# Kernel optimization log

Measured on AMD Instinct MI355X. Metric: run time of the kernel, lower is better.

The kernel has to match this reference:

```python
import jax, jax.numpy as jnp
import numpy as np

B, L = 32, 64
VOCAB, EMB, HID, MEM, NVAL = 32000, 256, 512, 256, 1024
NSLOTS, KTOP = 4096, 16
DEQ_ITERS, RELAX = 8, 0.5
DECAY, MEM_SCALE = 0.997, 1.0
HIDDEN = 1024  # max(128, 2*HID)


def _norm(x):
    # torch F.normalize: x / max(||x||, eps)
    return x / jnp.maximum(jnp.linalg.norm(x, axis=-1, keepdims=True), 1e-12)


def setup_inputs() -> dict:
    key = jax.random.key(0)
    ks = jax.random.split(key, 20)
    def gn(k, shape, scale):
        return jax.random.normal(k, shape, jnp.float32) * scale
    inp = {}
    inp['tokens'] = jax.random.randint(ks[0], (B, L), 0, VOCAB)
    inp['key_ids'] = jax.random.randint(ks[1], (B,), 0, NVAL)
    inp['write_pos'] = jax.random.randint(ks[2], (B,), 0, L // 2)
    inp['query_pos'] = jax.random.randint(ks[3], (B,), L // 2, L)
    inp['value_ids'] = jax.random.randint(ks[4], (B,), 0, NVAL)
    inp['embed_W'] = gn(ks[5], (VOCAB, EMB), 1.0)
    inp['key_W'] = gn(ks[6], (NVAL, MEM), 0.1)
    inp['value_W'] = gn(ks[7], (NVAL, MEM), 0.1)
    din = HID + EMB + MEM
    inp['u_W1'] = gn(ks[8], (din, HIDDEN), din ** -0.5)
    inp['u_b1'] = jnp.zeros((HIDDEN,), jnp.float32)
    inp['u_W2'] = gn(ks[9], (HIDDEN, HID), HIDDEN ** -0.5)
    inp['u_b2'] = jnp.zeros((HID,), jnp.float32)
    inp['l_Wi'] = gn(ks[10], (HID, HID), HID ** -0.5)
    inp['l_Wh'] = gn(ks[11], (HID, HID), HID ** -0.5)
    inp['l_b'] = jnp.zeros((HID,), jnp.float32)
    inp['l_Wti'] = gn(ks[12], (HID, HID), HID ** -0.5)
    inp['l_Wth'] = gn(ks[13], (HID, HID), HID ** -0.5)
    inp['l_bt'] = jnp.zeros((HID,), jnp.float32)
    inp['h0'] = jnp.zeros((HID,), jnp.float32)
    inp['z2v_W'] = gn(ks[14], (2 * HID, MEM), (2 * HID) ** -0.5)
    inp['z2v_b'] = jnp.zeros((MEM,), jnp.float32)
    inp['logit_scale_raw'] = jnp.asarray(2.0, jnp.float32)
    inp['slot_keys'] = _norm(gn(ks[15], (NSLOTS, MEM), 1.0))
    return inp


def _forward(tokens, key_ids, write_pos, query_pos, embed_W, key_W, value_W,
             u_W1, u_b1, u_W2, u_b2, l_Wi, l_Wh, l_b, l_Wti, l_Wth, l_bt,
             h0, z2v_W, z2v_b, logit_scale_raw, slot_keys):
    scale = jax.nn.softplus(logit_scale_raw) + 1e-3
    V_proto = _norm(value_W)                              # [NVAL, MEM]
    # Memory ops are non-differentiable in the original (detach + no_grad writes)
    kv = jax.lax.stop_gradient(_norm(key_W[key_ids]))     # [B, MEM]
    sk = jax.lax.stop_gradient(slot_keys)                 # [NSLOTS, MEM]

    x_seq = jnp.swapaxes(embed_W[tokens], 0, 1)           # [L, B, EMB]
    t_idx = jnp.arange(L)
    mw_seq = t_idx[:, None] == write_pos[None, :]         # [L, B]
    mq_seq = t_idx[:, None] == query_pos[None, :]         # [L, B]

    # Slot addressing depends only on the (fixed per-sequence) key vectors,
    # so the top-k slot selection can be hoisted out of the time loop.
    top_s, top_i = jax.lax.top_k(kv @ sk.T, KTOP)         # [B, KTOP]
    w_slot = jax.nn.softmax(top_s, axis=-1)               # [B, KTOP]

    def mem_read(M):
        return jnp.einsum('bk,bkd->bd', w_slot, M[top_i])  # gather [B,KTOP,MEM]

    def mem_write(M, vals, mask):
        wm = w_slot * mask[:, None].astype(M.dtype)
        contrib = jnp.zeros_like(M).at[top_i.reshape(-1)].add(
            (wm[..., None] * vals[:, None, :]).reshape(-1, MEM))
        decay_t = jnp.where(mask.any(), DECAY, 1.0)       # decay only on write events
        return decay_t * M + contrib

    def step(carry, xs):
        z, h, M, lm, lp = carry
        x_t, mw, mq = xs
        # mem_into_deq: non-diff memory read is injected only at query steps
        v_t = mem_read(M) * mq[:, None].astype(x_t.dtype) * MEM_SCALE
        # DEQ: damped fixed-point iteration z <- (1-r) z + r f(z)
        for _ in range(DEQ_ITERS):
            inp = jnp.concatenate([z, x_t, v_t], axis=-1)
            f = z + jnp.tanh(inp @ u_W1 + u_b1) @ u_W2 + u_b2
            z = (1.0 - RELAX) * z + RELAX * f
        # Liquid cell: time-constant gated relaxation toward tanh candidate
        g = jnp.tanh(z @ l_Wi + h @ l_Wh + l_b)
        tau = jax.nn.softplus(z @ l_Wti + h @ l_Wth + l_bt) + 1.0
        h = h + (g - h) / tau
        v_pred = _norm(jnp.concatenate([z, h], axis=-1) @ z2v_W + z2v_b)
        M = mem_write(M, jax.lax.stop_gradient(v_pred), mw)
        v_mem = mem_read(M)
        lm = jnp.where(mq[:, None], scale * (_norm(v_mem) @ V_proto.T), lm)
        lp = jnp.where(mq[:, None], scale * (v_pred @ V_proto.T), lp)
        return (z, h, M, lm, lp), None

    z0 = jnp.zeros((B, HID), jnp.float32)
    h_init = jnp.broadcast_to(h0, (B, HID))
    M0 = jnp.zeros((NSLOTS, MEM), jnp.float32)
    lm0 = jnp.zeros((B, NVAL), jnp.float32)
    lp0 = jnp.zeros((B, NVAL), jnp.float32)
    carry, _ = jax.lax.scan(step, (z0, h_init, M0, lm0, lp0), (x_seq, mw_seq, mq_seq))
    return carry[3]  # logits_main [B, NVAL]


def reference(tokens, key_ids, write_pos, query_pos, value_ids, embed_W, key_W,
              value_W, u_W1, u_b1, u_W2, u_b2, l_Wi, l_Wh, l_b, l_Wti, l_Wth,
              l_bt, h0, z2v_W, z2v_b, logit_scale_raw, slot_keys):
    # value_ids only feeds auxiliary losses in the original; logits_main does not use it.
    return _forward(tokens, key_ids, write_pos, query_pos, embed_W, key_W, value_W,
                    u_W1, u_b1, u_W2, u_b2, l_Wi, l_Wh, l_b, l_Wti, l_Wth, l_bt,
                    h0, z2v_W, z2v_b, logit_scale_raw, slot_keys)
```

## Files before the change

### kernel.cpp

```cpp
#include <hip/hip_runtime.h>
#include <math.h>


#define NGRP 8
#define WPG  32

#define OF_SCALE  0
#define OF_DFAC   32
#define OF_RNV    64
#define OF_TOPW   1088
#define OF_SCORES 1600
#define OF_Z      132672
#define OF_CP     198208
#define OF_G      230976
#define OF_TAU    247360
#define OF_H      263744
#define OF_ZS     280128
#define OF_HS     296512
#define OF_M      312896
#define OF_W1ZT   1361472
#define OF_W1XT   1885760
#define OF_W2T    2147904
#define OF_LWIT   2672192
#define OF_LWHT   2934336
#define OF_LWTIT  3196480
#define OF_LWTHT  3458624

__device__ __forceinline__ float softplusf_(float x){ return x > 20.f ? x : log1pf(expf(x)); }

__device__ __forceinline__ float cldf(const float* p){
  return __hip_atomic_load(p, __ATOMIC_RELAXED, __HIP_MEMORY_SCOPE_AGENT);
}
__device__ __forceinline__ void cstf(float* p, float v){
  __hip_atomic_store(p, v, __ATOMIC_RELAXED, __HIP_MEMORY_SCOPE_AGENT);
}

__device__ __forceinline__ void lbar(int* flags, int w, int& epoch){
  asm volatile("s_waitcnt vmcnt(0)" ::: "memory");
  __syncthreads();
  epoch++;
  if (threadIdx.x == 0)
    __hip_atomic_store(&flags[w], epoch, __ATOMIC_RELAXED, __HIP_MEMORY_SCOPE_AGENT);
  if (threadIdx.x < 32){
    while (__hip_atomic_load(&flags[threadIdx.x], __ATOMIC_RELAXED,
                             __HIP_MEMORY_SCOPE_AGENT) < epoch)
      __builtin_amdgcn_s_sleep(1);
  }
  asm volatile("" ::: "memory");
  __syncthreads();
}

__global__ void __launch_bounds__(256) emma_tr(const float* src, float* dst,
                                               int shift, int total)
{
  const int R = total >> shift;
  const int cmask = (1 << shift) - 1;
  for (int idx = blockIdx.x*256 + threadIdx.x; idx < total; idx += gridDim.x*256){
    int r = idx >> shift, c = idx & cmask;
    dst[(size_t)c * R + r] = src[idx];
  }
}

__global__ void __launch_bounds__(256) emma_k1a(
    const int* key_ids, const int* write_pos,
    const float* key_W, const float* value_W, const float* slot_keys,
    const float* lsr, int* wsI, float* wsF)
{
  const int wg = blockIdx.x, tid = threadIdx.x;
  if (wg < 256) {
    const int b = wg >> 3, chunk = wg & 7;
    __shared__ __align__(16) float s_kv[256];
    __shared__ float red[256];
    float v = key_W[key_ids[b]*256 + tid];
    red[tid] = v*v; __syncthreads();
    for (int st=128; st; st>>=1){ if (tid<st) red[tid]+=red[tid+st]; __syncthreads(); }
    float inv = 1.f/fmaxf(sqrtf(red[0]), 1e-12f);
    s_kv[tid] = v*inv;
    __syncthreads();
    const int lane = tid & 63, wv = tid >> 6;
    float4 kv4 = *(const float4*)(s_kv + lane*4);
    for (int slot = chunk*512 + wv; slot < chunk*512 + 512; slot += 4){
      float4 sk = *(const float4*)(slot_keys + (size_t)slot*256 + lane*4);
      float p = kv4.x*sk.x + kv4.y*sk.y + kv4.z*sk.z + kv4.w*sk.w;
      #pragma unroll
      for (int m=32;m;m>>=1) p += __shfl_xor(p, m, 64);
      if (lane==0) wsF[OF_SCORES + b*4096 + slot] = p;
    }
  } else if (wg < 320) {
    const int j = wg - 256;
    for (int i=tid;i<16384;i+=256) wsF[OF_M + j*16384 + i] = 0.f;
  } else if (wg < 324) {
    const int row = (wg-320)*256 + tid;
    float ss=0.f; const float* r = value_W + (size_t)row*256;
    for (int k=0;k<256;k++){ float x=r[k]; ss += x*x; }
    wsF[OF_RNV + row] = 1.f/fmaxf(sqrtf(ss), 1e-12f);
  } else {
    for (int i=tid;i<2048;i+=256) wsI[i]=0;
    __shared__ int pres[32];
    if (tid<32){ int p=0; for (int bb=0;bb<32;bb++) if (write_pos[bb]==tid) p=1; pres[tid]=p; }
    __syncthreads();
    if (tid<32){
      int wp = write_pos[tid]; float f=1.f;
      for (int s=wp+1;s<32;s++) if (pres[s]) f *= 0.997f;
      wsF[OF_DFAC + tid] = f;
    }
    if (tid==0) wsF[OF_SCALE] = softplusf_(lsr[0]) + 1e-3f;
  }
}

__global__ void __launch_bounds__(256) emma_k1b(int* wsI, float* wsF)
{
  const int b = blockIdx.x, tid = threadIdx.x;
  __shared__ float s_sc[4096];
  __shared__ float s_rv[256]; __shared__ int s_ri[256];
  __shared__ float s_tv[16];
  for (int n=tid;n<4096;n+=256) s_sc[n] = wsF[OF_SCORES + b*4096 + n];
  __syncthreads();
  for (int j=0;j<16;j++){
    float bv = -3.0e38f; int bi = 0x7fffffff;
    for (int n=tid;n<4096;n+=256){
      float v = s_sc[n];
      if (v > bv || (v == bv && n < bi)) { bv=v; bi=n; }
    }
    s_rv[tid]=bv; s_ri[tid]=bi; __syncthreads();
    for (int st=128; st; st>>=1){
      if (tid<st){
        float v2=s_rv[tid+st]; int i2=s_ri[tid+st];
        if (v2 > s_rv[tid] || (v2==s_rv[tid] && i2 < s_ri[tid])) { s_rv[tid]=v2; s_ri[tid]=i2; }
      }
      __syncthreads();
    }
    if (tid==0){
      s_tv[j] = s_rv[0];
      wsI[2048 + b*16 + j] = s_ri[0];
      s_sc[s_ri[0]] = -3.0e38f;
    }
    __syncthreads();
  }
  if (tid==0){
    float mx = s_tv[0], sum=0.f, w[16];
    for (int j=0;j<16;j++){ w[j]=expf(s_tv[j]-mx); sum+=w[j]; }
    for (int j=0;j<16;j++) wsF[OF_TOPW + b*16 + j] = w[j]/sum;
  }
}

__global__ void __launch_bounds__(256, 1) emma_k2(
    const int* tokens, const int* write_pos,
    const float* embed_W, const float* u_b1, const float* u_b2,
    const float* l_b, const float* l_bt, const float* h0,
    int* wsI, float* wsF)
{
  const int g = blockIdx.x & 7;
  const int w = blockIdx.x >> 3;
  const int tid = threadIdx.x;
  int* flags = wsI + g*32;
  int epoch = 0;

  float* Z  = wsF + OF_Z;
  float* CP = wsF + OF_CP;
  float* G  = wsF + OF_G;
  float* TA = wsF + OF_TAU;
  float* H  = wsF + OF_H;
  float* ZS = wsF + OF_ZS;
  float* HS = wsF + OF_HS;

  __shared__ __align__(16) float4 ldsA[32*129];
  __shared__ __align__(16) float4 ldsB[4096];
  __shared__ __align__(16) float zstage[4*520];
  __shared__ __align__(16) float tl[4*36];

  {
    const float* gA = wsF + OF_W1ZT + (size_t)(w*32)*512;
    const float* gB = wsF + OF_W2T;
    for (int idx4 = tid; idx4 < 4096; idx4 += 256){
      { int ci = idx4 >> 7, j = idx4 & 127;
        ldsA[ci*129 + j] = *(const float4*)(gA + (size_t)ci*512 + 4*j); }
      { int j4 = idx4 >> 9, c2 = idx4 & 511;
        ldsB[idx4] = *(const float4*)(gB + (size_t)c2*1024 + w*32 + 4*j4); }
    }
  }

  const int rA  = tid >> 5;
  const int bA  = g*4 + (rA & 3);
  const int ciA = tid & 31;
  const int cA  = w*32 + ciA;
  const int r3  = tid >> 6;
  const int c2l = tid & 63;
  const int rot = w & 7;
  const int kh  = w >> 4;
  float bh[8];
  #pragma unroll
  for (int cco=0;cco<8;cco++){
    int cc = (cco + rot) & 7;
    bh[cco] = 0.5f*u_b2[c2l + (cc<<6)];
  }
  float zp[8] = {0.f,0.f,0.f,0.f,0.f,0.f,0.f,0.f};

  if (w < 16) {
    int idx = w*256 + tid;
    if (idx < 2048) cstf(&Z[g*2048 + idx], 0.f);
    else { int i2=idx-2048; int r=i2>>9, c=i2&511; cstf(&H[(g*4+r)*512 + c], h0[c]); }
  } else {
    { int idx = (w-16)*256 + tid;
      if (idx < 2048) cstf(&Z[16384 + g*2048 + idx], 0.f); }
    int r = tid>>6, b = g*4+r;
    int c = (w-16)*64 + (tid&63);
    int tok = tokens[b*64 + 0];
    const float* xr = embed_W + (size_t)tok*256;
    const float* wc = wsF + OF_W1XT + (size_t)c*256;
    float a0=0,a1=0,a2=0,a3=0;
    #pragma unroll 4
    for (int k=0;k<256;k+=4){
      float4 xv = *(const float4*)(xr + k);
      float4 wv = *(const float4*)(wc + k);
      a0 += xv.x*wv.x; a1 += xv.y*wv.y; a2 += xv.z*wv.z; a3 += xv.w*wv.w;
    }
    cstf(&CP[b*1024 + c], u_b1[c] + ((a0+a1)+(a2+a3)));
  }
  lbar(flags, w, epoch);

  for (int s=0;s<32;s++){
    float cpv = (tid < 128) ? cldf(&CP[bA*1024 + cA]) : 0.f;
    for (int i=0;i<8;i++){
      float* zc = Z + (i&1)*16384;
      float* zn = Z + ((i&1)^1)*16384;
      #pragma unroll
      for (int k=0;k<8;k++){
        int idx = k*256 + tid;
        zstage[(idx>>9)*520 + (idx&511)] = cldf(&zc[g*2048 + idx]);
      }
      __syncthreads();
      if (tid < 128) {
        const float4* wc4 = ldsA + ciA*129;
        const float*  zr  = zstage + rA*520;
        float a0=0,a1=0,a2=0,a3=0;
        #pragma unroll 8
        for (int j=0;j<128;j++){
          float4 wv = wc4[j];
          float4 zv = *(const float4*)(zr + 4*j);
          a0 += zv.x*wv.x; a1 += zv.y*wv.y; a2 += zv.z*wv.z; a3 += zv.w*wv.w;
        }
        tl[rA*36 + ciA] = tanhf(cpv + (a0+a1)+(a2+a3));
      } else {
        if (i == 0 && w < 16 && s >= 1) {
          int idx = w*128 + (tid-128);
          int r = idx>>9, c2 = idx&511, b = g*4+r;
          float gv = tanhf(cldf(&G[b*512+c2]));
          float tv = softplusf_(cldf(&TA[b*512+c2])) + 1.0f;
          float hv = cldf(&H[b*512+c2]);
          float hn = hv + (gv - hv)/tv;
          cstf(&H[b*512+c2], hn);
          if (write_pos[b] == s-1) {
            cstf(&ZS[b*512+c2], zstage[r*520 + c2]);
            cstf(&HS[b*512+c2], hn);
          }
        } else if (i <= 1 && w >= 16 && s+1 < 32) {
          int e = i*2048 + (w-16)*128 + (tid-128);
          int r = e>>10, c = e&1023, b = g*4+r;
          int tok = tokens[b*64 + s+1];
          const float* xr = embed_W + (size_t)tok*256;
          const float* wc = wsF + OF_W1XT + (size_t)c*256;
          float a0=0,a1=0,a2=0,a3=0;
          #pragma unroll 4
          for (int k=0;k<256;k+=4){
            float4 xv = *(const float4*)(xr + k);
            float4 wv = *(const float4*)(wc + k);
            a0 += xv.x*wv.x; a1 += xv.y*wv.y; a2 += xv.z*wv.z; a3 += xv.w*wv.w;
          }
          cstf(&CP[b*1024 + c], u_b1[c] + ((a0+a1)+(a2+a3)));
        } else if (i == 7) {
          int idx = w*128 + (tid-128);
          if (idx < 2048){ int r=idx>>9, c=idx&511; cstf(&G[(g*4+r)*512+c], l_b[c]); }
          else { int i2=idx-2048; int r=i2>>9, c=i2&511; cstf(&TA[(g*4+r)*512+c], l_bt[c]); }
        }
      }
      __syncthreads();
      {
        const float* trow = tl + r3*36;
        float4 tvv[8];
        #pragma unroll
        for (int j4=0;j4<8;j4++) tvv[j4] = *(const float4*)(trow + 4*j4);
        float* zrow = &zn[(g*4+r3)*512];
        #pragma unroll
        for (int cco=0;cco<8;cco++){
          int cc = (cco + rot) & 7;
          int c2 = c2l + (cc<<6);
          const float4* wrow = ldsB + c2;
          float acc = 0.f;
          #pragma unroll
          for (int j4=0;j4<8;j4++){
            float4 wv = wrow[j4*512];
            float4 tv = tvv[j4];
            acc += tv.x*wv.x + tv.y*wv.y + tv.z*wv.z + tv.w*wv.w;
          }
          float zi = zstage[r3*520 + c2];
          float val = 0.5f*acc + (zi - zp[cco] + bh[cco]) * 0.03125f;
          zp[cco] = zi;
          atomicAdd(&zrow[c2], val);
        }
      }
      lbar(flags, w, epoch);
    }
    #pragma unroll
    for (int k=0;k<8;k++){
      int idx = k*256 + tid; int r = idx>>9, c = idx&511;
      const float* src = (kh==0) ? &Z[g*2048 + idx] : &H[g*2048 + idx];
      zstage[r*520 + c] = cldf(src);
    }
    __syncthreads();
    {
      int sub = tid>>7, l = tid&127;
      int r = l>>5, b = g*4+r;
      int c2 = (w&15)*32 + (l&31);
      const float* inrow = zstage + r*520;
      const float* Wc = (sub ? (kh==0 ? wsF+OF_LWTIT : wsF+OF_LWTHT)
                             : (kh==0 ? wsF+OF_LWIT  : wsF+OF_LWHT)) + (size_t)c2*512;
      float a0=0,a1=0,a2=0,a3=0;
      #pragma unroll 8
      for (int k=0;k<512;k+=4){
        float4 iv = *(const float4*)(inrow + k);
        float4 wv = *(const float4*)(Wc + k);
        a0 += iv.x*wv.x; a1 += iv.y*wv.y; a2 += iv.z*wv.z; a3 += iv.w*wv.w;
      }
      atomicAdd(sub ? &TA[b*512+c2] : &G[b*512+c2], (a0+a1)+(a2+a3));
    }
    lbar(flags, w, epoch);
  }
  if (w < 16 && tid >= 128) {
    int idx = w*128 + (tid-128);
    int r = idx>>9, c2 = idx&511, b = g*4+r;
    float gv = tanhf(cldf(&G[b*512+c2]));
    float tv = softplusf_(cldf(&TA[b*512+c2])) + 1.0f;
    float hv = cldf(&H[b*512+c2]);
    float hn = hv + (gv - hv)/tv;
    if (write_pos[b] == 31) {
      cstf(&ZS[b*512+c2], cldf(&Z[b*512+c2]));
      cstf(&HS[b*512+c2], hn);
    }
  }
}

__global__ void __launch_bounds__(256) emma_k3(const float* z2v_W, const float* z2v_b,
                                               int* wsI, float* wsF)
{
  const int b = blockIdx.x, c = threadIdx.x;
  const float* zs = wsF + OF_ZS + b*512;
  const float* hs = wsF + OF_HS + b*512;
  float acc = z2v_b[c];
  for (int k=0;k<512;k++) acc += zs[k]*z2v_W[k*256 + c];
  for (int k=0;k<512;k++) acc += hs[k]*z2v_W[(512+k)*256 + c];
  __shared__ float red[256];
  red[c]=acc*acc; __syncthreads();
  for (int st=128; st; st>>=1){ if (c<st) red[c]+=red[c+st]; __syncthreads(); }
  float inv = 1.f/fmaxf(sqrtf(red[0]),1e-12f);
  float vp = acc*inv;
  float f = wsF[OF_DFAC + b];
  for (int j=0;j<16;j++){
    int slot = wsI[2048 + b*16 + j];
    float wj = wsF[OF_TOPW + b*16 + j];
    atomicAdd(&wsF[OF_M + (size_t)slot*256 + c], f*wj*vp);
  }
}

__global__ void __launch_bounds__(256) emma_k4(const float* value_W, int* wsI, float* wsF,
                                               float* out)
{
  const int b = blockIdx.x, c = threadIdx.x;
  float m = 0.f;
  for (int j=0;j<16;j++){
    int slot = wsI[2048 + b*16 + j];
    m += wsF[OF_TOPW + b*16 + j] * wsF[OF_M + (size_t)slot*256 + c];
  }
  __shared__ float red[256];
  __shared__ float vn[256];
  red[c]=m*m; __syncthreads();
  for (int st=128; st; st>>=1){ if (c<st) red[c]+=red[c+st]; __syncthreads(); }
  float inv = 1.f/fmaxf(sqrtf(red[0]),1e-12f);
  vn[c] = m*inv;
  __syncthreads();
  float scale = wsF[OF_SCALE];
  for (int q=0;q<4;q++){
    int val = q*256 + c;
    const float* row = value_W + (size_t)val*256;
    float d0=0,d1=0,d2=0,d3=0;
    #pragma unroll 4
    for (int k=0;k<256;k+=4){
      float4 rv = *(const float4*)(row + k);
      d0 += vn[k+0]*rv.x; d1 += vn[k+1]*rv.y; d2 += vn[k+2]*rv.z; d3 += vn[k+3]*rv.w;
    }
    out[b*1024 + val] = scale * wsF[OF_RNV + val] * ((d0+d1)+(d2+d3));
  }
}

extern "C" void kernel_launch(void* const* d_in, const int* in_sizes, int n_in,
                              void* d_out, int out_size, void* d_ws, size_t ws_size,
                              hipStream_t stream)
{
  const int*   tokens    = (const int*)  d_in[0];
  const int*   key_ids   = (const int*)  d_in[1];
  const int*   write_pos = (const int*)  d_in[2];
  const float* embed_W   = (const float*)d_in[5];
  const float* key_W     = (const float*)d_in[6];
  const float* value_W   = (const float*)d_in[7];
  const float* u_W1      = (const float*)d_in[8];
  const float* u_b1      = (const float*)d_in[9];
  const float* u_W2      = (const float*)d_in[10];
  const float* u_b2      = (const float*)d_in[11];
  const float* l_Wi      = (const float*)d_in[12];
  const float* l_Wh      = (const float*)d_in[13];
  const float* l_b       = (const float*)d_in[14];
  const float* l_Wti     = (const float*)d_in[15];
  const float* l_Wth     = (const float*)d_in[16];
  const float* l_bt      = (const float*)d_in[17];
  const float* h0        = (const float*)d_in[18];
  const float* z2v_W     = (const float*)d_in[19];
  const float* z2v_b     = (const float*)d_in[20];
  const float* lsr       = (const float*)d_in[21];
  const float* slot_keys = (const float*)d_in[22];

  int*   wsI = (int*)d_ws;
  float* wsF = (float*)((char*)d_ws + 16384);
  float* out = (float*)d_out;

  hipLaunchKernelGGL(emma_k1a, dim3(325), dim3(256), 0, stream,
                     key_ids, write_pos, key_W, value_W, slot_keys, lsr, wsI, wsF);
  hipLaunchKernelGGL(emma_k1b, dim3(32), dim3(256), 0, stream, wsI, wsF);
  hipLaunchKernelGGL(emma_tr, dim3(512), dim3(256), 0, stream, u_W1,            wsF+OF_W1ZT, 10, 512*1024);
  hipLaunchKernelGGL(emma_tr, dim3(512), dim3(256), 0, stream, u_W1 + 512*1024, wsF+OF_W1XT, 10, 256*1024);
  hipLaunchKernelGGL(emma_tr, dim3(512), dim3(256), 0, stream, u_W2,            wsF+OF_W2T,   9, 1024*512);
  hipLaunchKernelGGL(emma_tr, dim3(512), dim3(256), 0, stream, l_Wi,            wsF+OF_LWIT,  9, 512*512);
  hipLaunchKernelGGL(emma_tr, dim3(512), dim3(256), 0, stream, l_Wh,            wsF+OF_LWHT,  9, 512*512);
  hipLaunchKernelGGL(emma_tr, dim3(512), dim3(256), 0, stream, l_Wti,           wsF+OF_LWTIT, 9, 512*512);
  hipLaunchKernelGGL(emma_tr, dim3(512), dim3(256), 0, stream, l_Wth,           wsF+OF_LWTHT, 9, 512*512);
  {
    void* args[] = { (void*)&tokens, (void*)&write_pos, (void*)&embed_W,
                     (void*)&u_b1, (void*)&u_b2, (void*)&l_b, (void*)&l_bt, (void*)&h0,
                     (void*)&wsI, (void*)&wsF };
    hipLaunchCooperativeKernel(reinterpret_cast<void*>(emma_k2), dim3(256), dim3(256),
                               args, 0, stream);
  }
  hipLaunchKernelGGL(emma_k3, dim3(32), dim3(256), 0, stream, z2v_W, z2v_b, wsI, wsF);
  hipLaunchKernelGGL(emma_k4, dim3(32), dim3(256), 0, stream, value_W, wsI, wsF, out);
}
```

Before: 3.457 ms.

## Replace atomic split-K second layer with exchanged hidden activations and output ownership

```diff
diff --git a/kernel.cpp b/kernel.cpp
--- a/kernel.cpp
+++ b/kernel.cpp
@@ -11,6 +11,7 @@
 #define OF_TOPW   1088
 #define OF_SCORES 1600
 #define OF_Z      132672
+#define OF_T      165440
 #define OF_CP     198208
 #define OF_G      230976
 #define OF_TAU    247360
@@ -157,6 +158,7 @@
   int epoch = 0;
 
   float* Z  = wsF + OF_Z;
+  float* T  = wsF + OF_T;
   float* CP = wsF + OF_CP;
   float* G  = wsF + OF_G;
   float* TA = wsF + OF_TAU;
@@ -165,18 +167,19 @@
   float* HS = wsF + OF_HS;
 
   __shared__ __align__(16) float4 ldsA[32*129];
-  __shared__ __align__(16) float4 ldsB[4096];
-  __shared__ __align__(16) float zstage[4*520];
-  __shared__ __align__(16) float tl[4*36];
+  __shared__ __align__(16) float  ldsB2[16*1028];
+  __shared__ __align__(16) float  zstage[4*520];
+  __shared__ __align__(16) float  tstage[4*1032];
+  __shared__ float redB[256];
 
   {
     const float* gA = wsF + OF_W1ZT + (size_t)(w*32)*512;
-    const float* gB = wsF + OF_W2T;
+    const float* gB = wsF + OF_W2T  + (size_t)(w*16)*1024;
     for (int idx4 = tid; idx4 < 4096; idx4 += 256){
       { int ci = idx4 >> 7, j = idx4 & 127;
         ldsA[ci*129 + j] = *(const float4*)(gA + (size_t)ci*512 + 4*j); }
-      { int j4 = idx4 >> 9, c2 = idx4 & 511;
-        ldsB[idx4] = *(const float4*)(gB + (size_t)c2*1024 + w*32 + 4*j4); }
+      { int c = idx4 >> 8, j = idx4 & 255;
+        *(float4*)(ldsB2 + c*1028 + 4*j) = *(const float4*)(gB + (size_t)c*1024 + 4*j); }
     }
   }
 
@@ -184,25 +187,17 @@
   const int bA  = g*4 + (rA & 3);
   const int ciA = tid & 31;
   const int cA  = w*32 + ciA;
-  const int r3  = tid >> 6;
-  const int c2l = tid & 63;
-  const int rot = w & 7;
+  const int qB  = tid >> 6;
+  const int rB  = (tid >> 4) & 3;
+  const int cB  = tid & 15;
   const int kh  = w >> 4;
-  float bh[8];
-  #pragma unroll
-  for (int cco=0;cco<8;cco++){
-    int cc = (cco + rot) & 7;
-    bh[cco] = 0.5f*u_b2[c2l + (cc<<6)];
-  }
-  float zp[8] = {0.f,0.f,0.f,0.f,0.f,0.f,0.f,0.f};
+  const float b2v = u_b2[w*16 + cB];
 
   if (w < 16) {
     int idx = w*256 + tid;
     if (idx < 2048) cstf(&Z[g*2048 + idx], 0.f);
     else { int i2=idx-2048; int r=i2>>9, c=i2&511; cstf(&H[(g*4+r)*512 + c], h0[c]); }
   } else {
-    { int idx = (w-16)*256 + tid;
-      if (idx < 2048) cstf(&Z[16384 + g*2048 + idx], 0.f); }
     int r = tid>>6, b = g*4+r;
     int c = (w-16)*64 + (tid&63);
     int tok = tokens[b*64 + 0];
@@ -240,7 +235,7 @@
           float4 zv = *(const float4*)(zr + 4*j);
           a0 += zv.x*wv.x; a1 += zv.y*wv.y; a2 += zv.z*wv.z; a3 += zv.w*wv.w;
         }
-        tl[rA*36 + ciA] = tanhf(cpv + (a0+a1)+(a2+a3));
+        cstf(&T[bA*1024 + cA], tanhf(cpv + (a0+a1)+(a2+a3)));
       } else {
         if (i == 0 && w < 16 && s >= 1) {
           int idx = w*128 + (tid-128);
@@ -274,30 +269,30 @@
           else { int i2=idx-2048; int r=i2>>9, c=i2&511; cstf(&TA[(g*4+r)*512+c], l_bt[c]); }
         }
       }
+      lbar(flags, w, epoch);
+      #pragma unroll
+      for (int k=0;k<16;k++){
+        int idx = k*256 + tid;
+        tstage[(idx>>10)*1032 + (idx&1023)] = cldf(&T[g*4096 + idx]);
+      }
       __syncthreads();
       {
-        const float* trow = tl + r3*36;
-        float4 tvv[8];
-        #pragma unroll
-        for (int j4=0;j4<8;j4++) tvv[j4] = *(const float4*)(trow + 4*j4);
-        float* zrow = &zn[(g*4+r3)*512];
-        #pragma unroll
-        for (int cco=0;cco<8;cco++){
-          int cc = (cco + rot) & 7;
-          int c2 = c2l + (cc<<6);
-          const float4* wrow = ldsB + c2;
-          float acc = 0.f;
-          #pragma unroll
-          for (int j4=0;j4<8;j4++){
-            float4 wv = wrow[j4*512];
-            float4 tv = tvv[j4];
-            acc += tv.x*wv.x + tv.y*wv.y + tv.z*wv.z + tv.w*wv.w;
-          }
-          float zi = zstage[r3*520 + c2];
-          float val = 0.5f*acc + (zi - zp[cco] + bh[cco]) * 0.03125f;
-          zp[cco] = zi;
-          atomicAdd(&zrow[c2], val);
+        const float* trow = tstage + rB*1032 + qB*256;
+        const float* wrow = ldsB2 + cB*1028 + qB*256;
+        float a0=0,a1=0,a2=0,a3=0;
+        #pragma unroll 8
+        for (int j=0;j<64;j++){
+          float4 tv = *(const float4*)(trow + 4*j);
+          float4 wv = *(const float4*)(wrow + 4*j);
+          a0 += tv.x*wv.x; a1 += tv.y*wv.y; a2 += tv.z*wv.z; a3 += tv.w*wv.w;
         }
+        redB[tid] = (a0+a1)+(a2+a3);
+      }
+      __syncthreads();
+      if (tid < 64){
+        float sum = redB[tid] + redB[tid+64] + redB[tid+128] + redB[tid+192];
+        int c2 = w*16 + cB;
+        cstf(&zn[(g*4+rB)*512 + c2], zstage[rB*520 + c2] + 0.5f*(sum + b2v));
       }
       lbar(flags, w, epoch);
     }
```

Result: slower. 4.658 ms (+34.7%).
